# Kernel optimization log

Hardware: AMD Instinct MI355X
Metric: run time of the kernel (lower is better)

The kernel has to match this reference:

```python
import jax, jax.numpy as jnp
import numpy as np

NEG_SLOPE = 0.2
EPS = 1e-6
K = 16


def vec_lna(x, Wf, Wd):
    # x: (B, Cin, 3, ...). Vector-neuron linear + VN-LeakyReLU.
    p = jnp.einsum('oc,bc...->bo...', Wf, x)          # features (B, Cout, 3, ...)
    d = jnp.einsum('oc,bc...->bo...', Wd, x)          # directions (B, Cd, 3, ...), Cd=Cout or 1 (shared)
    dot = jnp.sum(p * d, axis=2, keepdims=True)
    dsq = jnp.sum(d * d, axis=2, keepdims=True)
    p_ref = p - (dot / (dsq + EPS)) * d               # reflect negative part onto hyperplane
    return NEG_SLOPE * p + (1.0 - NEG_SLOPE) * jnp.where(dot >= 0, p, p_ref)


def knn_idx_fn(pts, k):
    # pts: (B, N, 3) -> (B, N, k) indices of k nearest neighbors (incl. self)
    sq = jnp.sum(pts * pts, axis=-1)                  # (B, N)
    d2 = sq[:, :, None] + sq[:, None, :] - 2.0 * jnp.einsum('bnd,bmd->bnm', pts, pts)
    _, idx = jax.lax.top_k(-d2, k)                    # smallest distances
    return idx


def graph_feature(x, idx):
    # x: (B, C, 3, N), idx: (B, N, k) -> (B, 2C, 3, N, k)
    nb = jax.vmap(lambda xb, ib: xb[:, :, ib])(x, idx)  # (B, C, 3, N, k)
    xc = x[..., None]
    return jnp.concatenate([nb - xc, jnp.broadcast_to(xc, nb.shape)], axis=1)


def _winit(key, co, ci):
    return jax.random.normal(key, (co, ci), dtype=jnp.float32) * np.sqrt(2.0 / ci).astype(np.float32)


def setup_inputs() -> dict:
    key = jax.random.key(0)
    ks = jax.random.split(key, 16)
    B, N = 4, 2048
    x = jax.random.normal(ks[0], (B, 3, N), dtype=jnp.float32)
    return {
        'x': x,
        'w1f': _winit(ks[1], 16, 2),   'w1d': _winit(ks[2], 16, 2),
        'w2f': _winit(ks[3], 32, 32),  'w2d': _winit(ks[4], 32, 32),
        'w3f': _winit(ks[5], 64, 64),  'w3d': _winit(ks[6], 64, 64),
        'w4f': _winit(ks[7], 128, 128),'w4d': _winit(ks[8], 128, 128),
        'wcf': _winit(ks[9], 128, 240),'wcd': _winit(ks[10], 1, 240),   # shared nonlinearity -> 1 dir channel
        'wi1f': _winit(ks[11], 128, 256), 'wi1d': _winit(ks[12], 128, 256),
        'wi2f': _winit(ks[13], 256, 128), 'wi2d': _winit(ks[14], 256, 128),
    }


def reference(x, w1f, w1d, w2f, w2d, w3f, w3d, w4f, w4d, wcf, wcd, wi1f, wi1d, wi2f, wi2d):
    # x: (B, 3, N)
    pts = jnp.transpose(x, (0, 2, 1))                 # (B, N, 3)
    idx = knn_idx_fn(pts, K)                          # (B, N, K) -- fixed graph (use_dg=False)
    h = x[:, None]                                    # (B, 1, 3, N)
    h = vec_lna(graph_feature(h, idx), w1f, w1d)
    x1 = h.mean(axis=-1)                              # (B, 16, 3, N)
    h = vec_lna(graph_feature(x1, idx), w2f, w2d)
    x2 = h.mean(axis=-1)                              # (B, 32, 3, N)
    h = vec_lna(graph_feature(x2, idx), w3f, w3d)
    x3 = h.mean(axis=-1)                              # (B, 64, 3, N)
    h = vec_lna(graph_feature(x3, idx), w4f, w4d)
    x4 = h.mean(axis=-1)                              # (B, 128, 3, N)
    xc = vec_lna(jnp.concatenate([x1, x2, x3, x4], axis=1), wcf, wcd)  # (B, 128, 3, N)
    xm = jnp.broadcast_to(xc.mean(axis=-1, keepdims=True), xc.shape)
    xcat = jnp.concatenate([xc, xm], axis=1)          # (B, 256, 3, N)
    x0 = vec_lna(vec_lna(xcat, wi1f, wi1d), wi2f, wi2d)
    inv = jnp.sum(xcat * x0, axis=2)                  # (B, 256, N) rotation-invariant features
    return inv
```

## Files before the change

### kernel.cpp

```cpp
#include <hip/hip_runtime.h>
#include <hip/hip_fp16.h>

#define NPTS  2048
#define BATCH 4
#define NBP   8192
#define MROWS 24576
#define KNN_K 16

typedef short bf16x8 __attribute__((ext_vector_type(8)));
typedef float f32x4  __attribute__((ext_vector_type(4)));

static __device__ __forceinline__ void split_bf16(float a, unsigned short& h, unsigned short& l)
{
    unsigned u = __float_as_uint(a);
    unsigned hr = (u + 0x7FFFu + ((u >> 16) & 1u)) & 0xFFFF0000u;
    h = (unsigned short)(hr >> 16);
    float rem = a - __uint_as_float(hr);
    unsigned v = __float_as_uint(rem);
    l = (unsigned short)((v + 0x7FFFu + ((v >> 16) & 1u)) >> 16);
}

static __device__ __forceinline__ float bf2(unsigned short h, unsigned short l)
{
    return __uint_as_float((unsigned)h << 16) + __uint_as_float((unsigned)l << 16);
}

static __device__ __forceinline__ float lna_scale(float dot, float dsq)
{
    return (dot < 0.f) ? 0.8f * dot * __builtin_amdgcn_rcpf(dsq + 1e-6f) : 0.f;
}

static __device__ __forceinline__ unsigned long long shfl_xor_u64(unsigned long long v, int mask)
{
    unsigned lo = (unsigned)v, hi = (unsigned)(v >> 32);
    lo = (unsigned)__shfl_xor((int)lo, mask, 64);
    hi = (unsigned)__shfl_xor((int)hi, mask, 64);
    return ((unsigned long long)hi << 32) | lo;
}

static __device__ __forceinline__ int xcd_swizzle(int i, int G)
{
    int batch  = (i >> 1) & 3;
    int within = ((i >> 3) << 1) | (i & 1);
    return batch * (G >> 2) + within;
}

static __device__ __forceinline__ float wbig_val(const float* __restrict__ Wf,
                                                 const float* __restrict__ Wd,
                                                 int j, int c, int O, int C)
{
    if (j < 2 * O) {
        int o = j >> 1;
        return (j & 1) ? Wd[o * 2 * C + c] : Wf[o * 2 * C + c];
    }
    int o = (j - 2 * O) >> 1;
    return (j & 1) ? (Wd[o * 2 * C + C + c] - Wd[o * 2 * C + c])
                   : (Wf[o * 2 * C + C + c] - Wf[o * 2 * C + c]);
}

static __device__ __forceinline__ int frag_ix(int r, int c, int RB)
{
    return (((c >> 5) * RB + (r >> 4)) * 64 + ((c >> 3) & 3) * 16 + (r & 15)) * 8 + (c & 7);
}

#define PC0 1572864
#define PC1 (PC0 + 4096)
#define PC2 (PC1 + 8192)
#define PC3 (PC2 + 32768)
#define PC4 (PC3 + 49152)
#define PC5 (PC4 + 32768)
#define PC6 (PC5 + 65536)
#define KNN_BLOCKS (NBP / 4)
#define PREP_BLOCKS (PC6 / 256)

__global__ __launch_bounds__(256) void prep_knn_kernel(
    const float* __restrict__ x, int* __restrict__ idx,
    __half* __restrict__ AH, float* __restrict__ AG,
    const float* __restrict__ w1f, const float* __restrict__ w1d,
    const float* __restrict__ w2f, const float* __restrict__ w2d,
    unsigned short* __restrict__ Wb2h, unsigned short* __restrict__ Wb2l,
    const float* __restrict__ w3f, const float* __restrict__ w3d,
    unsigned short* __restrict__ Wb3h, unsigned short* __restrict__ Wb3l,
    const float* __restrict__ w4f, const float* __restrict__ w4d,
    unsigned short* __restrict__ Wb4h, unsigned short* __restrict__ Wb4l,
    const float* __restrict__ wcf, const float* __restrict__ wcd,
    unsigned short* __restrict__ Wch, unsigned short* __restrict__ Wcl,
    const float* __restrict__ wi1f, const float* __restrict__ wi1d,
    unsigned short* __restrict__ Wi1h, unsigned short* __restrict__ Wi1l,
    const float* __restrict__ wi2f, const float* __restrict__ wi2d,
    unsigned short* __restrict__ Wi2h, unsigned short* __restrict__ Wi2l)
{
    __shared__ unsigned ksh[4][64 * 34];
    if (blockIdx.x < KNN_BLOCKS) {
        const int t  = threadIdx.x & 63;
        const int wq = threadIdx.x >> 6;
        const int bn = blockIdx.x * 4 + wq;
        const int b = bn >> 11;
        const int n = bn & (NPTS - 1);
        const float* xb = x + b * 3 * NPTS;
        const float qx = xb[n], qy = xb[NPTS + n], qz = xb[2 * NPTS + n];
        const float sqn = fmaf(qz, qz, fmaf(qy, qy, qx * qx));
        unsigned* ks = &ksh[wq][t * 34];

        unsigned gm[4];
        int ga[4];
#pragma unroll
        for (int g = 0; g < 4; g++) {
            unsigned kk[8];
#pragma unroll
            for (int j = 0; j < 8; j++) {
                const int i = g * 8 + j;
                const int m = (i << 6) + t;
                float mx = xb[m], my = xb[NPTS + m], mz = xb[2 * NPTS + m];
                float sqm = fmaf(mz, mz, fmaf(my, my, mx * mx));
                float dt  = fmaf(qz, mz, fmaf(qy, my, qx * mx));
                float d2  = sqn + sqm - 2.0f * dt;
                unsigned u = __float_as_uint(d2);
                u ^= (u & 0x80000000u) ? 0xFFFFFFFFu : 0x80000000u;
                kk[j] = u;
            }
            *(uint2*)&ks[g * 8 + 0] = make_uint2(kk[0], kk[1]);
            *(uint2*)&ks[g * 8 + 2] = make_uint2(kk[2], kk[3]);
            *(uint2*)&ks[g * 8 + 4] = make_uint2(kk[4], kk[5]);
            *(uint2*)&ks[g * 8 + 6] = make_uint2(kk[6], kk[7]);
            unsigned bg = kk[0];
            int ba = g * 8;
#pragma unroll
            for (int j = 1; j < 8; j++) {
                if (kk[j] < bg) { bg = kk[j]; ba = g * 8 + j; }
            }
            gm[g] = bg; ga[g] = ba;
        }
        unsigned lm = gm[0];
        int il = ga[0];
#pragma unroll
        for (int g = 1; g < 4; g++) if (gm[g] < lm) { lm = gm[g]; il = ga[g]; }

        unsigned long long pk = ((unsigned long long)lm << 32) | (unsigned)((il << 6) | t);
        int res = -1;
        for (int r = 0; r < KNN_K; r++) {
            unsigned long long w = pk;
#pragma unroll
            for (int off = 32; off > 0; off >>= 1) {
                unsigned long long o = shfl_xor_u64(w, off);
                w = (o < w) ? o : w;
            }
            if (t == r) res = (int)(w & 0xFFFFFFFFull);

            if (pk == w) {
                ks[il] = 0xFFFFFFFFu;
                const int g = il >> 3;
                unsigned bg = ks[g * 8];
                int ba = g * 8;
#pragma unroll
                for (int j = 1; j < 8; j++) {
                    unsigned kv = ks[g * 8 + j];
                    if (kv < bg) { bg = kv; ba = g * 8 + j; }
                }
                gm[g] = bg; ga[g] = ba;
                lm = gm[0]; il = ga[0];
#pragma unroll
                for (int g2 = 1; g2 < 4; g2++) if (gm[g2] < lm) { lm = gm[g2]; il = ga[g2]; }
                pk = ((unsigned long long)lm << 32) | (unsigned)((il << 6) | t);
            }
        }
        if (t < KNN_K) idx[bn * KNN_K + t] = res;
        return;
    }

    const int i = (blockIdx.x - KNN_BLOCKS) * 256 + threadIdx.x;
    if (i < PC0) {
        int o = i & 63;
        int row = i >> 6;
        int v = row % 3;
        int gp = row / 3;
        int b = gp >> 11;
        int n = gp & (NPTS - 1);
        float xv = x[(b * 3 + v) * NPTS + n];
        float wv = wbig_val(w1f, w1d, o, 0, 16, 1);
        float val = xv * wv;
        if (o < 32) AH[(size_t)row * 32 + o] = __float2half(val);
        else        AG[(size_t)row * 32 + o - 32] = val;
    } else if (i < PC6) {
        float v = 0.f;
        unsigned short *ph, *pl;
        int ix;
        if (i < PC1) {
            ix = i - PC0;
            int c = ix & 31, j = ix >> 5;
            if (c < 16) v = wbig_val(w2f, w2d, j, c, 32, 16);
            ph = Wb2h; pl = Wb2l;
        } else if (i < PC2) {
            ix = i - PC1;
            int c = ix & 31, j = ix >> 5;
            v = wbig_val(w3f, w3d, j, c, 64, 32);
            ph = Wb3h; pl = Wb3l;
        } else if (i < PC3) {
            ix = i - PC2;
            int c = ix & 63, j = ix >> 6;
            v = wbig_val(w4f, w4d, j, c, 128, 64);
            ph = Wb4h; pl = Wb4l;
        } else if (i < PC4) {
            ix = i - PC3;
            int c = ix & 255, r = ix >> 8;
            if (c < 240) {
                if (r < 128) v = wcf[r * 240 + c];
                else if (r < 129) v = wcd[(r - 128) * 240 + c];
            }
            ph = Wch; pl = Wcl;
            ix = frag_ix(r, c, 12);
        } else if (i < PC5) {
            ix = i - PC4;
            int c = ix & 127, r = ix >> 7;
            if (r < 128) v = wi1f[r * 256 + c];
            else v = wi1d[(r - 128) * 256 + c];
            ph = Wi1h; pl = Wi1l;
            ix = frag_ix(r, c, 16);
        } else {
            ix = i - PC5;
            int c = ix & 127, r = ix >> 7;
            int o = r >> 1;
            v = (r & 1) ? wi2d[o * 128 + c] : wi2f[o * 128 + c];
            ph = Wi2h; pl = Wi2l;
            ix = frag_ix(r, c, 32);
        }
        unsigned short h, l;
        split_bf16(v, h, l);
        ph[ix] = h; pl[ix] = l;
    }
}

template <int OIN, int NF>
__global__ __launch_bounds__(256, 3) void edge_gemm_kernel(
    const __half* __restrict__ AHin, const float* __restrict__ AGin,
    const int* __restrict__ idx,
    unsigned short* __restrict__ X240h, unsigned short* __restrict__ X240l, int ooff,
    const unsigned short* __restrict__ Wh, const unsigned short* __restrict__ Wl,
    __half* __restrict__ OUTA, float* __restrict__ OUTG)
{
    constexpr int PTS = 16;
    constexpr int NC = NF * 64;
    constexpr int twoO = NC / 2;
    constexpr int LDW = 40;
    constexpr int CPT = OIN / 16;
    constexpr int twoOin = 2 * OIN;

    __shared__ unsigned short Xsh[48][32];
    __shared__ unsigned short Xsl[48][32];
    __shared__ unsigned short wbh[NC][LDW];
    __shared__ unsigned short wbl[NC][LDW];
    __shared__ int sIdx[PTS][KNN_K];

    const int lb = xcd_swizzle(blockIdx.x, gridDim.x);
    const int tid = threadIdx.x;

    for (int rr = tid; rr < NC; rr += 256) {
#pragma unroll
        for (int scc = 0; scc < 4; scc++) {
            *(uint4*)&wbh[rr][scc * 8] = *(const uint4*)(Wh + (size_t)rr * 32 + scc * 8);
            *(uint4*)&wbl[rr][scc * 8] = *(const uint4*)(Wl + (size_t)rr * 32 + scc * 8);
        }
    }
    for (int j = tid; j < PTS * KNN_K; j += 256)
        sIdx[j >> 4][j & 15] = idx[(lb * PTS + (j >> 4)) * KNN_K + (j & 15)];
    __syncthreads();

    const int op = tid & 15;
    const int pt = tid >> 4;
    const int gp = lb * PTS + pt;
    const int b = gp >> 11;
    const int rown = gp * 3;
    const int bbase = (b << 11) * 3;

    float cg[3][2 * CPT];
#pragma unroll
    for (int v = 0; v < 3; v++) {
        if constexpr (CPT == 2) {
            float4 c4 = *(const float4*)&AGin[(size_t)(rown + v) * twoOin + 4 * op];
            cg[v][0] = c4.x; cg[v][1] = c4.y; cg[v][2] = c4.z; cg[v][3] = c4.w;
        } else {
            float2 c2 = *(const float2*)&AGin[(size_t)(rown + v) * twoOin + 2 * op];
            cg[v][0] = c2.x; cg[v][1] = c2.y;
        }
    }
    float am[CPT][3];
#pragma unroll
    for (int c0 = 0; c0 < CPT; c0++) { am[c0][0] = 0.f; am[c0][1] = 0.f; am[c0][2] = 0.f; }

#pragma unroll 2
    for (int k = 0; k < KNN_K; k++) {
        const int m = sIdx[pt][k];
        const __half* base = AHin + (size_t)(bbase + m * 3) * twoOin + 2 * CPT * op;
        float e[3][2 * CPT];
#pragma unroll
        for (int v = 0; v < 3; v++) {
            if constexpr (CPT == 2) {
                uint2 u = *(const uint2*)(base + (size_t)v * twoOin);
                float2 x0 = __half22float2(*(__half2*)&u.x);
                float2 x1 = __half22float2(*(__half2*)&u.y);
                e[v][0] = x0.x; e[v][1] = x0.y; e[v][2] = x1.x; e[v][3] = x1.y;
            } else {
                unsigned u = *(const unsigned*)(base + (size_t)v * twoOin);
                float2 x0 = __half22float2(*(__half2*)&u);
                e[v][0] = x0.x; e[v][1] = x0.y;
            }
        }
#pragma unroll
        for (int c0 = 0; c0 < CPT; c0++) {
            float p0 = e[0][2 * c0] + cg[0][2 * c0], d0 = e[0][2 * c0 + 1] + cg[0][2 * c0 + 1];
            float p1 = e[1][2 * c0] + cg[1][2 * c0], d1 = e[1][2 * c0 + 1] + cg[1][2 * c0 + 1];
            float p2 = e[2][2 * c0] + cg[2][2 * c0], d2 = e[2][2 * c0 + 1] + cg[2][2 * c0 + 1];
            float dot = fmaf(p2, d2, fmaf(p1, d1, p0 * d0));
            float dsq = fmaf(d2, d2, fmaf(d1, d1, d0 * d0));
            float s = lna_scale(dot, dsq);
            am[c0][0] += fmaf(-s, d0, p0);
            am[c0][1] += fmaf(-s, d1, p1);
            am[c0][2] += fmaf(-s, d2, p2);
        }
    }

#pragma unroll
    for (int v = 0; v < 3; v++) {
#pragma unroll
        for (int c0 = 0; c0 < CPT; c0++) {
            const int ch = CPT * op + c0;
            unsigned short h, l;
            split_bf16(am[c0][v] * 0.0625f, h, l);
            Xsh[pt * 3 + v][ch] = h;
            Xsl[pt * 3 + v][ch] = l;
            const size_t ob = (size_t)(rown + v) * 256 + ooff + ch;
            X240h[ob] = h; X240l[ob] = l;
        }
        if constexpr (CPT == 1) {
            Xsh[pt * 3 + v][16 + op] = 0;
            Xsl[pt * 3 + v][16 + op] = 0;
        }
    }
    __syncthreads();

    const int lane = tid & 63;
    const int wv = tid >> 6;
    const int mr = lane & 15;
    const int q  = lane >> 4;

    f32x4 acc[3][NF];
#pragma unroll
    for (int a = 0; a < 3; a++)
#pragma unroll
        for (int c = 0; c < NF; c++) acc[a][c] = (f32x4){0.f, 0.f, 0.f, 0.f};

    bf16x8 ah[3], al[3], bh[NF], bl[NF];
#pragma unroll
    for (int mf = 0; mf < 3; mf++) {
        ah[mf] = *(const bf16x8*)&Xsh[mf * 16 + mr][q * 8];
        al[mf] = *(const bf16x8*)&Xsl[mf * 16 + mr][q * 8];
    }
#pragma unroll
    for (int nf = 0; nf < NF; nf++) {
        const int wr = wv * 16 * NF + nf * 16 + mr;
        bh[nf] = *(const bf16x8*)&wbh[wr][q * 8];
        bl[nf] = *(const bf16x8*)&wbl[wr][q * 8];
    }
#pragma unroll
    for (int mf = 0; mf < 3; mf++)
#pragma unroll
        for (int nf = 0; nf < NF; nf++) {
            acc[mf][nf] = __builtin_amdgcn_mfma_f32_16x16x32_bf16(ah[mf], bh[nf], acc[mf][nf], 0, 0, 0);
            acc[mf][nf] = __builtin_amdgcn_mfma_f32_16x16x32_bf16(ah[mf], bl[nf], acc[mf][nf], 0, 0, 0);
            acc[mf][nf] = __builtin_amdgcn_mfma_f32_16x16x32_bf16(al[mf], bh[nf], acc[mf][nf], 0, 0, 0);
        }

    const int rbase = lb * 48;
#pragma unroll
    for (int nf = 0; nf < NF; nf++) {
        const int col = wv * 16 * NF + nf * 16 + mr;
#pragma unroll
        for (int mf = 0; mf < 3; mf++)
#pragma unroll
            for (int i = 0; i < 4; i++) {
                const int row = rbase + mf * 16 + q * 4 + i;
                const float val = acc[mf][nf][i];
                if (col < twoO) OUTA[(size_t)row * twoO + col] = __float2half(val);
                else            OUTG[(size_t)row * twoO + col - twoO] = val;
            }
    }
}

__global__ __launch_bounds__(256) void gemm_mfma(
    const unsigned short* __restrict__ Xh, const unsigned short* __restrict__ Xl,
    int ldx, int xoff,
    const unsigned short* __restrict__ Wh, const unsigned short* __restrict__ Wl,
    float* __restrict__ OUT, int ldo, int Nout, int Kpad,
    __half* __restrict__ OUTA, float* __restrict__ OUTG, int twoO)
{
    __shared__ unsigned short Ws[2][64][56];
    const int tid = threadIdx.x;
    const int bm = blockIdx.x * 256;
    const int bo = blockIdx.y * 64;
    const int lane = tid & 63;
    const int wv = tid >> 6;
    const int mr = lane & 15;
    const int q  = lane >> 4;

    f32x4 acc[4][4];
#pragma unroll
    for (int a = 0; a < 4; a++)
#pragma unroll
        for (int c = 0; c < 4; c++) acc[a][c] = (f32x4){0.f, 0.f, 0.f, 0.f};

    const int wr = tid >> 2;
    const int sc = tid & 3;

    for (int k0 = 0; k0 < Kpad; k0 += 32) {
        {
            const uint4 vh = *(const uint4*)(Wh + (size_t)(bo + wr) * Kpad + k0 + sc * 8);
            const uint4 vl = *(const uint4*)(Wl + (size_t)(bo + wr) * Kpad + k0 + sc * 8);
            *(uint4*)&Ws[0][wr][sc * 8] = vh;
            *(uint4*)&Ws[1][wr][sc * 8] = vl;
        }
        __syncthreads();

        bf16x8 ah[4], al[4], bh[4], bl[4];
#pragma unroll
        for (int mf = 0; mf < 4; mf++) {
            const size_t xrow = (size_t)(bm + wv * 64 + mf * 16 + mr) * ldx + xoff + k0 + q * 8;
            ah[mf] = *(const bf16x8*)(Xh + xrow);
            al[mf] = *(const bf16x8*)(Xl + xrow);
        }
#pragma unroll
        for (int nf = 0; nf < 4; nf++) {
            bh[nf] = *(const bf16x8*)&Ws[0][nf * 16 + mr][q * 8];
            bl[nf] = *(const bf16x8*)&Ws[1][nf * 16 + mr][q * 8];
        }
#pragma unroll
        for (int mf = 0; mf < 4; mf++)
#pragma unroll
            for (int nf = 0; nf < 4; nf++) {
                acc[mf][nf] = __builtin_amdgcn_mfma_f32_16x16x32_bf16(ah[mf], bh[nf], acc[mf][nf], 0, 0, 0);
                acc[mf][nf] = __builtin_amdgcn_mfma_f32_16x16x32_bf16(ah[mf], bl[nf], acc[mf][nf], 0, 0, 0);
                acc[mf][nf] = __builtin_amdgcn_mfma_f32_16x16x32_bf16(al[mf], bh[nf], acc[mf][nf], 0, 0, 0);
            }
        __syncthreads();
    }

    if (OUTA) {
#pragma unroll
        for (int nf = 0; nf < 4; nf++) {
            const int col = bo + nf * 16 + mr;
            if (col < twoO) {
#pragma unroll
                for (int mf = 0; mf < 4; mf++)
#pragma unroll
                    for (int i = 0; i < 4; i++) {
                        const int row = bm + wv * 64 + mf * 16 + q * 4 + i;
                        OUTA[(size_t)row * twoO + col] = __float2half(acc[mf][nf][i]);
                    }
            } else {
#pragma unroll
                for (int mf = 0; mf < 4; mf++)
#pragma unroll
                    for (int i = 0; i < 4; i++) {
                        const int row = bm + wv * 64 + mf * 16 + q * 4 + i;
                        OUTG[(size_t)row * twoO + col - twoO] = acc[mf][nf][i];
                    }
            }
        }
    } else {
#pragma unroll
        for (int nf = 0; nf < 4; nf++) {
            const int col = bo + nf * 16 + mr;
            if (col < Nout) {
#pragma unroll
                for (int mf = 0; mf < 4; mf++)
#pragma unroll
                    for (int i = 0; i < 4; i++) {
                        const int row = bm + wv * 64 + mf * 16 + q * 4 + i;
                        OUT[(size_t)row * ldo + col] = acc[mf][nf][i];
                    }
            }
        }
    }
}

template <int O, int PT>
__global__ __launch_bounds__(256, 6) void edge_kernel(const __half* __restrict__ AH,
                                                      const float* __restrict__ AG,
                                                      const int* __restrict__ idx,
                                                      unsigned short* __restrict__ outh,
                                                      unsigned short* __restrict__ outl,
                                                      int ooff)
{
    constexpr int TP = O / 2;
    constexpr int twoO = 2 * O;
    const int lb = xcd_swizzle(blockIdx.x, gridDim.x);
    const int tid = threadIdx.x;
    const int op = tid % TP;
    const int pt = tid / TP;
    const int gp = lb * PT + pt;
    const int b = gp >> 11;
    __shared__ int sIdx[PT][KNN_K];
    for (int j = tid; j < PT * KNN_K; j += 256)
        sIdx[j >> 4][j & 15] = idx[(lb * PT + (j >> 4)) * KNN_K + (j & 15)];
    __syncthreads();
    const int rown = gp * 3;
    const float4 c0 = *(const float4*)&AG[(size_t)(rown + 0) * twoO + 4 * op];
    const float4 c1 = *(const float4*)&AG[(size_t)(rown + 1) * twoO + 4 * op];
    const float4 c2 = *(const float4*)&AG[(size_t)(rown + 2) * twoO + 4 * op];
    float ax0 = 0.f, ax1 = 0.f, ax2 = 0.f;
    float ay0 = 0.f, ay1 = 0.f, ay2 = 0.f;
    const int bbase = (b << 11) * 3;
#pragma unroll 2
    for (int k = 0; k < KNN_K; k++) {
        int m = sIdx[pt][k];
        const __half* base = AH + (size_t)(bbase + m * 3) * twoO + 4 * op;
        uint2 u0 = *(const uint2*)(base);
        uint2 u1 = *(const uint2*)(base + twoO);
        uint2 u2 = *(const uint2*)(base + 2 * twoO);
        float2 e0 = __half22float2(*(__half2*)&u0.x);
        float2 f0 = __half22float2(*(__half2*)&u0.y);
        float2 e1 = __half22float2(*(__half2*)&u1.x);
        float2 f1 = __half22float2(*(__half2*)&u1.y);
        float2 e2 = __half22float2(*(__half2*)&u2.x);
        float2 f2 = __half22float2(*(__half2*)&u2.y);
        {
            float p0 = e0.x + c0.x, d0 = e0.y + c0.y;
            float p1 = e1.x + c1.x, d1 = e1.y + c1.y;
            float p2 = e2.x + c2.x, d2 = e2.y + c2.y;
            float dot = fmaf(p2, d2, fmaf(p1, d1, p0 * d0));
            float dsq = fmaf(d2, d2, fmaf(d1, d1, d0 * d0));
            float s = lna_scale(dot, dsq);
            ax0 += fmaf(-s, d0, p0);
            ax1 += fmaf(-s, d1, p1);
            ax2 += fmaf(-s, d2, p2);
        }
        {
            float p0 = f0.x + c0.z, d0 = f0.y + c0.w;
            float p1 = f1.x + c1.z, d1 = f1.y + c1.w;
            float p2 = f2.x + c2.z, d2 = f2.y + c2.w;
            float dot = fmaf(p2, d2, fmaf(p1, d1, p0 * d0));
            float dsq = fmaf(d2, d2, fmaf(d1, d1, d0 * d0));
            float s = lna_scale(dot, dsq);
            ay0 += fmaf(-s, d0, p0);
            ay1 += fmaf(-s, d1, p1);
            ay2 += fmaf(-s, d2, p2);
        }
    }
    float rx[3] = { ax0 * 0.0625f, ax1 * 0.0625f, ax2 * 0.0625f };
    float ry[3] = { ay0 * 0.0625f, ay1 * 0.0625f, ay2 * 0.0625f };
#pragma unroll
    for (int v = 0; v < 3; v++) {
        unsigned short hx, lx, hy, ly;
        split_bf16(rx[v], hx, lx);
        split_bf16(ry[v], hy, ly);
        const size_t ob = (size_t)(rown + v) * 256 + ooff + 2 * op;
        *(unsigned*)(outh + ob) = (unsigned)hx | ((unsigned)hy << 16);
        *(unsigned*)(outl + ob) = (unsigned)lx | ((unsigned)ly << 16);
    }
}

#define EW_LDX 136
#define EW_LDT 133
__global__ __launch_bounds__(256, 4) void edge_wc_kernel(
    const __half* __restrict__ AHin, const float* __restrict__ AGin,
    const int* __restrict__ idx,
    const unsigned short* __restrict__ Xh, const unsigned short* __restrict__ Xl,
    const unsigned short* __restrict__ Wh, const unsigned short* __restrict__ Wl,
    unsigned short* __restrict__ oh, unsigned short* __restrict__ ol,
    float* __restrict__ part2)
{
    __shared__ __align__(16) char smem[48 * EW_LDX * 2 * 2];
    unsigned short (*x4h)[EW_LDX] = (unsigned short (*)[EW_LDX])smem;
    unsigned short (*x4l)[EW_LDX] = (unsigned short (*)[EW_LDX])(smem + 48 * EW_LDX * 2);
    float* tb = (float*)smem;
    __shared__ int sIdx[16][KNN_K];

    const int lb = xcd_swizzle(blockIdx.x, gridDim.x);
    const int tid = threadIdx.x;

    for (int j = tid; j < 16 * KNN_K; j += 256)
        sIdx[j >> 4][j & 15] = idx[(lb * 16 + (j >> 4)) * KNN_K + (j & 15)];
    __syncthreads();

    {
        const int op = tid & 15;
        const int pt = tid >> 4;
        const int gp = lb * 16 + pt;
        const int b = gp >> 11;
        const int rown = gp * 3;
        const int bbase = (b << 11) * 3;

        float cg[3][16];
#pragma unroll
        for (int v = 0; v < 3; v++) {
            const float* ag = &AGin[(size_t)(rown + v) * 256 + 16 * op];
#pragma unroll
            for (int t = 0; t < 4; t++) {
                float4 c4 = *(const float4*)(ag + 4 * t);
                cg[v][4 * t + 0] = c4.x; cg[v][4 * t + 1] = c4.y;
                cg[v][4 * t + 2] = c4.z; cg[v][4 * t + 3] = c4.w;
            }
        }
        float am[8][3];
#pragma unroll
        for (int c0 = 0; c0 < 8; c0++) { am[c0][0] = 0.f; am[c0][1] = 0.f; am[c0][2] = 0.f; }

        for (int k = 0; k < KNN_K; k++) {
            const int m = sIdx[pt][k];
            const __half* base = AHin + (size_t)(bbase + m * 3) * 256 + 16 * op;
            unsigned uw[3][8];
#pragma unroll
            for (int v = 0; v < 3; v++) {
                uint4 a  = *(const uint4*)(base + (size_t)v * 256);
                uint4 bq = *(const uint4*)(base + (size_t)v * 256 + 8);
                uw[v][0] = a.x;  uw[v][1] = a.y;  uw[v][2] = a.z;  uw[v][3] = a.w;
                uw[v][4] = bq.x; uw[v][5] = bq.y; uw[v][6] = bq.z; uw[v][7] = bq.w;
            }
#pragma unroll
            for (int c0 = 0; c0 < 8; c0++) {
                float2 e0 = __half22float2(*(__half2*)&uw[0][c0]);
                float2 e1 = __half22float2(*(__half2*)&uw[1][c0]);
                float2 e2 = __half22float2(*(__half2*)&uw[2][c0]);
                float p0 = e0.x + cg[0][2 * c0], d0 = e0.y + cg[0][2 * c0 + 1];
                float p1 = e1.x + cg[1][2 * c0], d1 = e1.y + cg[1][2 * c0 + 1];
                float p2 = e2.x + cg[2][2 * c0], d2 = e2.y + cg[2][2 * c0 + 1];
                float dot = fmaf(p2, d2, fmaf(p1, d1, p0 * d0));
                float dsq = fmaf(d2, d2, fmaf(d1, d1, d0 * d0));
                float s = lna_scale(dot, dsq);
                am[c0][0] += fmaf(-s, d0, p0);
                am[c0][1] += fmaf(-s, d1, p1);
                am[c0][2] += fmaf(-s, d2, p2);
            }
        }
#pragma unroll
        for (int v = 0; v < 3; v++)
#pragma unroll
            for (int c0 = 0; c0 < 8; c0++) {
                unsigned short h, l;
                split_bf16(am[c0][v] * 0.0625f, h, l);
                x4h[pt * 3 + v][8 * op + c0] = h;
                x4l[pt * 3 + v][8 * op + c0] = l;
            }
    }
    __syncthreads();

    const int lane = tid & 63;
    const int wv = tid >> 6;
    const int mr = lane & 15;
    const int q  = lane >> 4;
    const int rbase = lb * 48;

    f32x4 acc[3][3];
#pragma unroll
    for (int a = 0; a < 3; a++)
#pragma unroll
        for (int c = 0; c < 3; c++) acc[a][c] = (f32x4){0.f, 0.f, 0.f, 0.f};

    for (int k0 = 0; k0 < 256; k0 += 32) {
        const int kb = k0 + q * 8;
        bf16x8 ah[3], al[3], bh[3], bl[3];
#pragma unroll
        for (int mf = 0; mf < 3; mf++) {
            const int row = mf * 16 + mr;
            if (kb >= 112) {
                if (kb >= 240) {
                    ah[mf] = (bf16x8){0, 0, 0, 0, 0, 0, 0, 0};
                    al[mf] = (bf16x8){0, 0, 0, 0, 0, 0, 0, 0};
                } else {
                    ah[mf] = *(const bf16x8*)&x4h[row][kb - 112];
                    al[mf] = *(const bf16x8*)&x4l[row][kb - 112];
                }
            } else {
                const size_t xr = (size_t)(rbase + row) * 256 + kb;
                ah[mf] = *(const bf16x8*)(Xh + xr);
                al[mf] = *(const bf16x8*)(Xl + xr);
            }
        }
#pragma unroll
        for (int nf = 0; nf < 3; nf++) {
            const size_t wri = (size_t)((((k0 >> 5) * 12) + wv * 3 + nf) * 64 + lane) * 8;
            bh[nf] = *(const bf16x8*)(Wh + wri);
            bl[nf] = *(const bf16x8*)(Wl + wri);
        }
#pragma unroll
        for (int mf = 0; mf < 3; mf++)
#pragma unroll
            for (int nf = 0; nf < 3; nf++) {
                acc[mf][nf] = __builtin_amdgcn_mfma_f32_16x16x32_bf16(ah[mf], bh[nf], acc[mf][nf], 0, 0, 0);
                acc[mf][nf] = __builtin_amdgcn_mfma_f32_16x16x32_bf16(ah[mf], bl[nf], acc[mf][nf], 0, 0, 0);
                acc[mf][nf] = __builtin_amdgcn_mfma_f32_16x16x32_bf16(al[mf], bh[nf], acc[mf][nf], 0, 0, 0);
            }
    }
    __syncthreads();

#pragma unroll
    for (int mf = 0; mf < 3; mf++)
#pragma unroll
        for (int nf = 0; nf < 3; nf++) {
            const int col = wv * 48 + nf * 16 + mr;
            if (col <= 128) {
#pragma unroll
                for (int i = 0; i < 4; i++)
                    tb[(mf * 16 + q * 4 + i) * EW_LDT + col] = acc[mf][nf][i];
            }
        }
    __syncthreads();

    const int bp0 = lb * 16;
    float vacc[3] = {0.f, 0.f, 0.f};
#pragma unroll
    for (int it = 0; it < 8; it++) {
        const int item = it * 256 + tid;
        const int o = item & 127;
        const int pt = item >> 7;
        float p[3], d[3];
#pragma unroll
        for (int v = 0; v < 3; v++) {
            const int r = pt * 3 + v;
            p[v] = tb[r * EW_LDT + o];
            d[v] = tb[r * EW_LDT + 128];
        }
        float dot = fmaf(p[2], d[2], fmaf(p[1], d[1], p[0] * d[0]));
        float dsq = fmaf(d[2], d[2], fmaf(d[1], d[1], d[0] * d[0]));
        float s = lna_scale(dot, dsq);
#pragma unroll
        for (int v = 0; v < 3; v++) {
            float val = fmaf(-s, d[v], p[v]);
            vacc[v] += val;
            unsigned short h, l;
            split_bf16(val, h, l);
            const size_t ob = ((size_t)(bp0 + pt) * 3 + v) * 128 + o;
            oh[ob] = h; ol[ob] = l;
        }
    }

    __syncthreads();
    tb[tid] = vacc[0]; tb[256 + tid] = vacc[1]; tb[512 + tid] = vacc[2];
    __syncthreads();
    if (tid < 128) {
#pragma unroll
        for (int v = 0; v < 3; v++)
            part2[(size_t)lb * 384 + v * 128 + tid] =
                tb[v * 256 + tid] + tb[v * 256 + tid + 128];
    }
}

__global__ __launch_bounds__(128) void xm_reduce_ym_kernel(
    const float* __restrict__ part2,
    unsigned short* __restrict__ xmh, unsigned short* __restrict__ xml,
    const float* __restrict__ wi1f, const float* __restrict__ wi1d,
    float* __restrict__ ym)
{
    __shared__ float xs[128];
    const int bv = blockIdx.x;
    const int b = bv / 3;
    const int v = bv % 3;
    const int o = threadIdx.x;
    float acc = 0.f;
    for (int i = 0; i < 128; i++)
        acc += part2[(size_t)(b * 128 + i) * 384 + v * 128 + o];
    const float m = acc * (1.f / 2048.f);
    unsigned short h, l;
    split_bf16(m, h, l);
    xmh[bv * 128 + o] = h;
    xml[bv * 128 + o] = l;
    xs[o] = m;
    __syncthreads();
#pragma unroll
    for (int half = 0; half < 2; half++) {
        const int oo = half * 128 + o;
        const float* wrow = (oo < 128) ? (wi1f + (size_t)oo * 256 + 128)
                                       : (wi1d + (size_t)(oo - 128) * 256 + 128);
        float s = 0.f;
        for (int c = 0; c < 128; c++) s = fmaf(wrow[c], xs[c], s);
        ym[(size_t)bv * 256 + oo] = s;
    }
}

#define QI_LDY  136
#define QI_LDT  257
#define QI_LDT2 67
__global__ __launch_bounds__(256, 2) void gemm_ii_kernel(
    const unsigned short* __restrict__ xch, const unsigned short* __restrict__ xcl,
    const unsigned short* __restrict__ W1h, const unsigned short* __restrict__ W1l,
    const unsigned short* __restrict__ W2h, const unsigned short* __restrict__ W2l,
    const unsigned short* __restrict__ xmh, const unsigned short* __restrict__ xml,
    const float* __restrict__ ym,
    float* __restrict__ out)
{
    __shared__ __align__(16) char regA[51456];
    __shared__ __align__(16) unsigned short y1h[48][QI_LDY];
    __shared__ __align__(16) unsigned short y1l[48][QI_LDY];
    float* tb = (float*)regA;

    const int tid = threadIdx.x;
    const int lane = tid & 63;
    const int wv = tid >> 6;
    const int mr = lane & 15;
    const int q  = lane >> 4;
    const int lb = blockIdx.x;
    const int bm = lb * 48;
    const int bb = (lb * 16) >> 11;

    f32x4 acc[3][4];
#pragma unroll
    for (int a = 0; a < 3; a++)
#pragma unroll
        for (int c = 0; c < 4; c++) acc[a][c] = (f32x4){0.f, 0.f, 0.f, 0.f};

    for (int k0 = 0; k0 < 128; k0 += 32) {
        bf16x8 ah[3], al[3];
#pragma unroll
        for (int mf = 0; mf < 3; mf++) {
            const size_t xr = (size_t)(bm + mf * 16 + mr) * 128 + k0 + q * 8;
            ah[mf] = *(const bf16x8*)(xch + xr);
            al[mf] = *(const bf16x8*)(xcl + xr);
        }
        const int ks = k0 >> 5;
#pragma unroll
        for (int nf = 0; nf < 4; nf++) {
            const size_t wi = (size_t)((ks * 16 + wv * 4 + nf) * 64 + lane) * 8;
            const bf16x8 bh = *(const bf16x8*)(W1h + wi);
            const bf16x8 bl = *(const bf16x8*)(W1l + wi);
#pragma unroll
            for (int mf = 0; mf < 3; mf++) {
                acc[mf][nf] = __builtin_amdgcn_mfma_f32_16x16x32_bf16(ah[mf], bh, acc[mf][nf], 0, 0, 0);
                acc[mf][nf] = __builtin_amdgcn_mfma_f32_16x16x32_bf16(ah[mf], bl, acc[mf][nf], 0, 0, 0);
                acc[mf][nf] = __builtin_amdgcn_mfma_f32_16x16x32_bf16(al[mf], bh, acc[mf][nf], 0, 0, 0);
            }
        }
    }

#pragma unroll
    for (int mf = 0; mf < 3; mf++)
#pragma unroll
        for (int nf = 0; nf < 4; nf++)
#pragma unroll
            for (int i = 0; i < 4; i++)
                tb[(size_t)(mf * 16 + q * 4 + i) * QI_LDT + wv * 64 + nf * 16 + mr] = acc[mf][nf][i];
    __syncthreads();

    {
        const int oo = tid & 127;
        float ymp[3], ymd[3];
#pragma unroll
        for (int v = 0; v < 3; v++) {
            ymp[v] = ym[(size_t)(bb * 3 + v) * 256 + oo];
            ymd[v] = ym[(size_t)(bb * 3 + v) * 256 + 128 + oo];
        }
#pragma unroll
        for (int it = 0; it < 8; it++) {
            const int item = it * 256 + tid;
            const int o = item & 127;
            const int pt = item >> 7;
            float p[3], d[3];
#pragma unroll
            for (int v = 0; v < 3; v++) {
                const int r = pt * 3 + v;
                p[v] = tb[(size_t)r * QI_LDT + o] + ymp[v];
                d[v] = tb[(size_t)r * QI_LDT + 128 + o] + ymd[v];
            }
            float dot = fmaf(p[2], d[2], fmaf(p[1], d[1], p[0] * d[0]));
            float dsq = fmaf(d[2], d[2], fmaf(d[1], d[1], d[0] * d[0]));
            float s = lna_scale(dot, dsq);
#pragma unroll
            for (int v = 0; v < 3; v++) {
                unsigned short h, l;
                split_bf16(fmaf(-s, d[v], p[v]), h, l);
                y1h[pt * 3 + v][o] = h;
                y1l[pt * 3 + v][o] = l;
            }
        }
    }
    __syncthreads();

    f32x4 acc2[3][8];
#pragma unroll
    for (int a = 0; a < 3; a++)
#pragma unroll
        for (int c = 0; c < 8; c++) acc2[a][c] = (f32x4){0.f, 0.f, 0.f, 0.f};

    for (int k0 = 0; k0 < 128; k0 += 32) {
        bf16x8 ah[3], al[3];
#pragma unroll
        for (int mf = 0; mf < 3; mf++) {
            ah[mf] = *(const bf16x8*)&y1h[mf * 16 + mr][k0 + q * 8];
            al[mf] = *(const bf16x8*)&y1l[mf * 16 + mr][k0 + q * 8];
        }
#pragma unroll
        for (int nf = 0; nf < 8; nf++) {
            const size_t wi = (size_t)((((k0 >> 5) * 32) + wv * 8 + nf) * 64 + lane) * 8;
            const bf16x8 bh = *(const bf16x8*)(W2h + wi);
            const bf16x8 bl = *(const bf16x8*)(W2l + wi);
#pragma unroll
            for (int mf = 0; mf < 3; mf++) {
                acc2[mf][nf] = __builtin_amdgcn_mfma_f32_16x16x32_bf16(ah[mf], bh, acc2[mf][nf], 0, 0, 0);
                acc2[mf][nf] = __builtin_amdgcn_mfma_f32_16x16x32_bf16(ah[mf], bl, acc2[mf][nf], 0, 0, 0);
                acc2[mf][nf] = __builtin_amdgcn_mfma_f32_16x16x32_bf16(al[mf], bh, acc2[mf][nf], 0, 0, 0);
            }
        }
    }

    float* wt = tb + wv * (48 * QI_LDT2);
#pragma unroll
    for (int hf = 0; hf < 2; hf++) {
        __syncthreads();
#pragma unroll
        for (int mf = 0; mf < 3; mf++)
#pragma unroll
            for (int nf2 = 0; nf2 < 4; nf2++)
#pragma unroll
                for (int i = 0; i < 4; i++)
                    wt[(mf * 16 + q * 4 + i) * QI_LDT2 + nf2 * 16 + mr] = acc2[mf][hf * 4 + nf2][i];
#pragma unroll
        for (int j = 0; j < 8; j++) {
            const int item = j * 64 + lane;
            const int ol = item & 31;
            const int pt = item >> 5;
            const int og = wv * 64 + hf * 32 + ol;
            const int gp = lb * 16 + pt;
            float p[3], d[3], xc[3];
#pragma unroll
            for (int v = 0; v < 3; v++) {
                p[v] = wt[(3 * pt + v) * QI_LDT2 + 2 * ol];
                d[v] = wt[(3 * pt + v) * QI_LDT2 + 2 * ol + 1];
                if (og < 128) {
                    const size_t ix = (size_t)(gp * 3 + v) * 128 + og;
                    xc[v] = bf2(xch[ix], xcl[ix]);
                } else {
                    const size_t ix = (size_t)(bb * 3 + v) * 128 + og - 128;
                    xc[v] = bf2(xmh[ix], xml[ix]);
                }
            }
            float dot = fmaf(p[2], d[2], fmaf(p[1], d[1], p[0] * d[0]));
            float dsq = fmaf(d[2], d[2], fmaf(d[1], d[1], d[0] * d[0]));
            float s = lna_scale(dot, dsq);
            float inv = 0.f;
#pragma unroll
            for (int v = 0; v < 3; v++)
                inv = fmaf(xc[v], fmaf(-s, d[v], p[v]), inv);
            out[((size_t)bb * 256 + og) * NPTS + (gp & (NPTS - 1))] = inv;
        }
    }
}

extern "C" void kernel_launch(void* const* d_in, const int* in_sizes, int n_in,
                              void* d_out, int out_size, void* d_ws, size_t ws_size,
                              hipStream_t stream)
{
    const float* x    = (const float*)d_in[0];
    const float* w1f  = (const float*)d_in[1];
    const float* w1d  = (const float*)d_in[2];
    const float* w2f  = (const float*)d_in[3];
    const float* w2d  = (const float*)d_in[4];
    const float* w3f  = (const float*)d_in[5];
    const float* w3d  = (const float*)d_in[6];
    const float* w4f  = (const float*)d_in[7];
    const float* w4d  = (const float*)d_in[8];
    const float* wcf  = (const float*)d_in[9];
    const float* wcd  = (const float*)d_in[10];
    const float* wi1f = (const float*)d_in[11];
    const float* wi1d = (const float*)d_in[12];
    const float* wi2f = (const float*)d_in[13];
    const float* wi2d = (const float*)d_in[14];
    float* out = (float*)d_out;

    float* F = (float*)d_ws;
    size_t off = 0;
    float* AG = F + off;                          off += (size_t)MROWS * 512;
    __half* AH = (__half*)(F + off);              off += (size_t)MROWS * 128;
    __half* AH2 = (__half*)(F + off);             off += (size_t)MROWS * 128;
    unsigned short* X240h = (unsigned short*)(F + off); off += (size_t)MROWS * 128;
    unsigned short* X240l = (unsigned short*)(F + off); off += (size_t)MROWS * 128;
    unsigned short* xc2h  = (unsigned short*)(F + off); off += (size_t)MROWS * 64;
    unsigned short* xc2l  = (unsigned short*)(F + off); off += (size_t)MROWS * 64;
    unsigned short* Wb2h = (unsigned short*)(F + off); off += 2048;
    unsigned short* Wb2l = (unsigned short*)(F + off); off += 2048;
    unsigned short* Wb3h = (unsigned short*)(F + off); off += 4096;
    unsigned short* Wb3l = (unsigned short*)(F + off); off += 4096;
    unsigned short* Wb4h = (unsigned short*)(F + off); off += 16384;
    unsigned short* Wb4l = (unsigned short*)(F + off); off += 16384;
    unsigned short* Wch  = (unsigned short*)(F + off); off += 24576;
    unsigned short* Wcl  = (unsigned short*)(F + off); off += 24576;
    unsigned short* Wi1h = (unsigned short*)(F + off); off += 32768;
    unsigned short* Wi1l = (unsigned short*)(F + off); off += 32768;
    unsigned short* Wi2h = (unsigned short*)(F + off); off += 32768;
    unsigned short* Wi2l = (unsigned short*)(F + off); off += 32768;
    float* part2 = F + off;                       off += (size_t)512 * 384;
    float* ym    = F + off;                       off += 12 * 256;
    unsigned short* xmph = (unsigned short*)(F + off); off += 768;
    unsigned short* xmpl = (unsigned short*)(F + off); off += 768;
    int* idx    = (int*)(F + off);                off += NBP * KNN_K;
    float* AG2 = AG + (size_t)MROWS * 256;

    prep_knn_kernel<<<KNN_BLOCKS + PREP_BLOCKS, 256, 0, stream>>>(
        x, idx, AH, AG, w1f, w1d,
        w2f, w2d, Wb2h, Wb2l, w3f, w3d, Wb3h, Wb3l, w4f, w4d, Wb4h, Wb4l,
        wcf, wcd, Wch, Wcl, wi1f, wi1d, Wi1h, Wi1l, wi2f, wi2d, Wi2h, Wi2l);

    const int GM = MROWS / 256;

    edge_gemm_kernel<16, 2><<<NBP / 16, 256, 0, stream>>>(
        AH, AG, idx, X240h, X240l, 0, Wb2h, Wb2l, AH2, AG2);
    edge_gemm_kernel<32, 4><<<NBP / 16, 256, 0, stream>>>(
        AH2, AG2, idx, X240h, X240l, 16, Wb3h, Wb3l, AH, AG);
    edge_kernel<64, 8><<<NBP / 8, 256, 0, stream>>>(AH, AG, idx, X240h, X240l, 48);
    gemm_mfma<<<dim3(GM, 8), 256, 0, stream>>>(X240h, X240l, 256, 48, Wb4h, Wb4l, nullptr, 0, 512, 64, AH2, AG2, 256);

    edge_wc_kernel<<<NBP / 16, 256, 0, stream>>>(AH2, AG2, idx, X240h, X240l,
                                                 Wch, Wcl, xc2h, xc2l, part2);

    xm_reduce_ym_kernel<<<BATCH * 3, 128, 0, stream>>>(part2, xmph, xmpl, wi1f, wi1d, ym);

    gemm_ii_kernel<<<MROWS / 48, 256, 0, stream>>>(xc2h, xc2l, Wi1h, Wi1l,
                                                   Wi2h, Wi2l, xmph, xmpl, ym, out);

    (void)in_sizes; (void)n_in; (void)out_size; (void)ws_size;
}
```

Measured before the change: 252.0 us.

## Fuse layer-3 edge aggregation with layer-4 projection GEMM into one kernel

Replaces the separate edge_kernel<64,8> and gemm_mfma launches with a single edge_gemm4_kernel. Each block aggregates 16 points' neighbor features into shared memory as split bf16 and then runs the 512-wide MFMA projection directly from LDS. The Wb4 weights are pre-laid-out in fragment order so each lane loads B fragments straight from global memory. This removes one launch and the global round-trip of the aggregated features before the GEMM. In exchange it raises register pressure (24 accumulators per lane, launch bounds of 2) and re-reads the weights from global memory in every block.

```diff
diff --git a/kernel.cpp b/kernel.cpp
--- a/kernel.cpp
+++ b/kernel.cpp
@@ -197,9 +197,10 @@
             ph = Wb3h; pl = Wb3l;
         } else if (i < PC3) {
             ix = i - PC2;
-            int c = ix & 63, j = ix >> 6;
-            v = wbig_val(w4f, w4d, j, c, 128, 64);
+            int c = ix & 63, r = ix >> 6;
+            v = wbig_val(w4f, w4d, r, c, 128, 64);
             ph = Wb4h; pl = Wb4l;
+            ix = frag_ix(r, c, 32);
         } else if (i < PC4) {
             ix = i - PC3;
             int c = ix & 255, r = ix >> 8;
@@ -386,175 +387,130 @@
     }
 }
 
-__global__ __launch_bounds__(256) void gemm_mfma(
-    const unsigned short* __restrict__ Xh, const unsigned short* __restrict__ Xl,
-    int ldx, int xoff,
+__global__ __launch_bounds__(256, 2) void edge_gemm4_kernel(
+    const __half* __restrict__ AHin, const float* __restrict__ AGin,
+    const int* __restrict__ idx,
+    unsigned short* __restrict__ X240h, unsigned short* __restrict__ X240l,
     const unsigned short* __restrict__ Wh, const unsigned short* __restrict__ Wl,
-    float* __restrict__ OUT, int ldo, int Nout, int Kpad,
-    __half* __restrict__ OUTA, float* __restrict__ OUTG, int twoO)
-{
-    __shared__ unsigned short Ws[2][64][56];
+    __half* __restrict__ OUTA, float* __restrict__ OUTG)
+{
+    __shared__ unsigned short Xsh[48][72];
+    __shared__ unsigned short Xsl[48][72];
+    __shared__ int sIdx[16][KNN_K];
+
+    const int lb = xcd_swizzle(blockIdx.x, gridDim.x);
     const int tid = threadIdx.x;
-    const int bm = blockIdx.x * 256;
-    const int bo = blockIdx.y * 64;
+
+    for (int j = tid; j < 16 * KNN_K; j += 256)
+        sIdx[j >> 4][j & 15] = idx[(lb * 16 + (j >> 4)) * KNN_K + (j & 15)];
+    __syncthreads();
+
+    {
+        const int op = tid & 15;
+        const int pt = tid >> 4;
+        const int gp = lb * 16 + pt;
+        const int b = gp >> 11;
+        const int rown = gp * 3;
+        const int bbase = (b << 11) * 3;
+
+        float cg[3][8];
+#pragma unroll
+        for (int v = 0; v < 3; v++) {
+            const float* ag = &AGin[(size_t)(rown + v) * 128 + 8 * op];
+            float4 c4a = *(const float4*)ag;
+            float4 c4b = *(const float4*)(ag + 4);
+            cg[v][0] = c4a.x; cg[v][1] = c4a.y; cg[v][2] = c4a.z; cg[v][3] = c4a.w;
+            cg[v][4] = c4b.x; cg[v][5] = c4b.y; cg[v][6] = c4b.z; cg[v][7] = c4b.w;
+        }
+        float am[4][3];
+#pragma unroll
+        for (int c0 = 0; c0 < 4; c0++) { am[c0][0] = 0.f; am[c0][1] = 0.f; am[c0][2] = 0.f; }
+
+        for (int k = 0; k < KNN_K; k++) {
+            const int m = sIdx[pt][k];
+            const __half* base = AHin + (size_t)(bbase + m * 3) * 128 + 8 * op;
+            unsigned uw[3][4];
+#pragma unroll
+            for (int v = 0; v < 3; v++) {
+                uint4 a = *(const uint4*)(base + (size_t)v * 128);
+                uw[v][0] = a.x; uw[v][1] = a.y; uw[v][2] = a.z; uw[v][3] = a.w;
+            }
+#pragma unroll
+            for (int c0 = 0; c0 < 4; c0++) {
+                float2 e0 = __half22float2(*(__half2*)&uw[0][c0]);
+                float2 e1 = __half22float2(*(__half2*)&uw[1][c0]);
+                float2 e2 = __half22float2(*(__half2*)&uw[2][c0]);
+                float p0 = e0.x + cg[0][2 * c0], d0 = e0.y + cg[0][2 * c0 + 1];
+                float p1 = e1.x + cg[1][2 * c0], d1 = e1.y + cg[1][2 * c0 + 1];
+                float p2 = e2.x + cg[2][2 * c0], d2 = e2.y + cg[2][2 * c0 + 1];
+                float dot = fmaf(p2, d2, fmaf(p1, d1, p0 * d0));
+                float dsq = fmaf(d2, d2, fmaf(d1, d1, d0 * d0));
+                float s = lna_scale(dot, dsq);
+                am[c0][0] += fmaf(-s, d0, p0);
+                am[c0][1] += fmaf(-s, d1, p1);
+                am[c0][2] += fmaf(-s, d2, p2);
+            }
+        }
+#pragma unroll
+        for (int v = 0; v < 3; v++)
+#pragma unroll
+            for (int c0 = 0; c0 < 4; c0++) {
+                const int ch = 4 * op + c0;
+                unsigned short h, l;
+                split_bf16(am[c0][v] * 0.0625f, h, l);
+                Xsh[pt * 3 + v][ch] = h;
+                Xsl[pt * 3 + v][ch] = l;
+                const size_t ob = (size_t)(rown + v) * 256 + 48 + ch;
+                X240h[ob] = h; X240l[ob] = l;
+            }
+    }
+    __syncthreads();
+
     const int lane = tid & 63;
     const int wv = tid >> 6;
     const int mr = lane & 15;
     const int q  = lane >> 4;
 
-    f32x4 acc[4][4];
-#pragma unroll
-    for (int a = 0; a < 4; a++)
-#pragma unroll
-        for (int c = 0; c < 4; c++) acc[a][c] = (f32x4){0.f, 0.f, 0.f, 0.f};
-
-    const int wr = tid >> 2;
-    const int sc = tid & 3;
-
-    for (int k0 = 0; k0 < Kpad; k0 += 32) {
-        {
-            const uint4 vh = *(const uint4*)(Wh + (size_t)(bo + wr) * Kpad + k0 + sc * 8);
-            const uint4 vl = *(const uint4*)(Wl + (size_t)(bo + wr) * Kpad + k0 + sc * 8);
-            *(uint4*)&Ws[0][wr][sc * 8] = vh;
-            *(uint4*)&Ws[1][wr][sc * 8] = vl;
-        }
-        __syncthreads();
-
-        bf16x8 ah[4], al[4], bh[4], bl[4];
-#pragma unroll
-        for (int mf = 0; mf < 4; mf++) {
-            const size_t xrow = (size_t)(bm + wv * 64 + mf * 16 + mr) * ldx + xoff + k0 + q * 8;
-            ah[mf] = *(const bf16x8*)(Xh + xrow);
-            al[mf] = *(const bf16x8*)(Xl + xrow);
-        }
-#pragma unroll
-        for (int nf = 0; nf < 4; nf++) {
-            bh[nf] = *(const bf16x8*)&Ws[0][nf * 16 + mr][q * 8];
-            bl[nf] = *(const bf16x8*)&Ws[1][nf * 16 + mr][q * 8];
-        }
-#pragma unroll
-        for (int mf = 0; mf < 4; mf++)
-#pragma unroll
-            for (int nf = 0; nf < 4; nf++) {
-                acc[mf][nf] = __builtin_amdgcn_mfma_f32_16x16x32_bf16(ah[mf], bh[nf], acc[mf][nf], 0, 0, 0);
-                acc[mf][nf] = __builtin_amdgcn_mfma_f32_16x16x32_bf16(ah[mf], bl[nf], acc[mf][nf], 0, 0, 0);
-                acc[mf][nf] = __builtin_amdgcn_mfma_f32_16x16x32_bf16(al[mf], bh[nf], acc[mf][nf], 0, 0, 0);
-            }
-        __syncthreads();
-    }
-
-    if (OUTA) {
-#pragma unroll
-        for (int nf = 0; nf < 4; nf++) {
-            const int col = bo + nf * 16 + mr;
-            if (col < twoO) {
-#pragma unroll
-                for (int mf = 0; mf < 4; mf++)
-#pragma unroll
-                    for (int i = 0; i < 4; i++) {
-                        const int row = bm + wv * 64 + mf * 16 + q * 4 + i;
-                        OUTA[(size_t)row * twoO + col] = __float2half(acc[mf][nf][i]);
-                    }
-            } else {
-#pragma unroll
-                for (int mf = 0; mf < 4; mf++)
-#pragma unroll
-                    for (int i = 0; i < 4; i++) {
-                        const int row = bm + wv * 64 + mf * 16 + q * 4 + i;
-                        OUTG[(size_t)row * twoO + col - twoO] = acc[mf][nf][i];
-                    }
-            }
-        }
-    } else {
-#pragma unroll
-        for (int nf = 0; nf < 4; nf++) {
-            const int col = bo + nf * 16 + mr;
-            if (col < Nout) {
-#pragma unroll
-                for (int mf = 0; mf < 4; mf++)
-#pragma unroll
-                    for (int i = 0; i < 4; i++) {
-                        const int row = bm + wv * 64 + mf * 16 + q * 4 + i;
-                        OUT[(size_t)row * ldo + col] = acc[mf][nf][i];
-                    }
-            }
-        }
-    }
-}
-
-template <int O, int PT>
-__global__ __launch_bounds__(256, 6) void edge_kernel(const __half* __restrict__ AH,
-                                                      const float* __restrict__ AG,
-                                                      const int* __restrict__ idx,
-                                                      unsigned short* __restrict__ outh,
-                                                      unsigned short* __restrict__ outl,
-                                                      int ooff)
-{
-    constexpr int TP = O / 2;
-    constexpr int twoO = 2 * O;
-    const int lb = xcd_swizzle(blockIdx.x, gridDim.x);
-    const int tid = threadIdx.x;
-    const int op = tid % TP;
-    const int pt = tid / TP;
-    const int gp = lb * PT + pt;
-    const int b = gp >> 11;
-    __shared__ int sIdx[PT][KNN_K];
-    for (int j = tid; j < PT * KNN_K; j += 256)
-        sIdx[j >> 4][j & 15] = idx[(lb * PT + (j >> 4)) * KNN_K + (j & 15)];
-    __syncthreads();
-    const int rown = gp * 3;
-    const float4 c0 = *(const float4*)&AG[(size_t)(rown + 0) * twoO + 4 * op];
-    const float4 c1 = *(const float4*)&AG[(size_t)(rown + 1) * twoO + 4 * op];
-    const float4 c2 = *(const float4*)&AG[(size_t)(rown + 2) * twoO + 4 * op];
-    float ax0 = 0.f, ax1 = 0.f, ax2 = 0.f;
-    float ay0 = 0.f, ay1 = 0.f, ay2 = 0.f;
-    const int bbase = (b << 11) * 3;
-#pragma unroll 2
-    for (int k = 0; k < KNN_K; k++) {
-        int m = sIdx[pt][k];
-        const __half* base = AH + (size_t)(bbase + m * 3) * twoO + 4 * op;
-        uint2 u0 = *(const uint2*)(base);
-        uint2 u1 = *(const uint2*)(base + twoO);
-        uint2 u2 = *(const uint2*)(base + 2 * twoO);
-        float2 e0 = __half22float2(*(__half2*)&u0.x);
-        float2 f0 = __half22float2(*(__half2*)&u0.y);
-        float2 e1 = __half22float2(*(__half2*)&u1.x);
-        float2 f1 = __half22float2(*(__half2*)&u1.y);
-        float2 e2 = __half22float2(*(__half2*)&u2.x);
-        float2 f2 = __half22float2(*(__half2*)&u2.y);
-        {
-            float p0 = e0.x + c0.x, d0 = e0.y + c0.y;
-            float p1 = e1.x + c1.x, d1 = e1.y + c1.y;
-            float p2 = e2.x + c2.x, d2 = e2.y + c2.y;
-            float dot = fmaf(p2, d2, fmaf(p1, d1, p0 * d0));
-            float dsq = fmaf(d2, d2, fmaf(d1, d1, d0 * d0));
-            float s = lna_scale(dot, dsq);
-            ax0 += fmaf(-s, d0, p0);
-            ax1 += fmaf(-s, d1, p1);
-            ax2 += fmaf(-s, d2, p2);
-        }
-        {
-            float p0 = f0.x + c0.z, d0 = f0.y + c0.w;
-            float p1 = f1.x + c1.z, d1 = f1.y + c1.w;
-            float p2 = f2.x + c2.z, d2 = f2.y + c2.w;
-            float dot = fmaf(p2, d2, fmaf(p1, d1, p0 * d0));
-            float dsq = fmaf(d2, d2, fmaf(d1, d1, d0 * d0));
-            float s = lna_scale(dot, dsq);
-            ay0 += fmaf(-s, d0, p0);
-            ay1 += fmaf(-s, d1, p1);
-            ay2 += fmaf(-s, d2, p2);
-        }
-    }
-    float rx[3] = { ax0 * 0.0625f, ax1 * 0.0625f, ax2 * 0.0625f };
-    float ry[3] = { ay0 * 0.0625f, ay1 * 0.0625f, ay2 * 0.0625f };
-#pragma unroll
-    for (int v = 0; v < 3; v++) {
-        unsigned short hx, lx, hy, ly;
-        split_bf16(rx[v], hx, lx);
-        split_bf16(ry[v], hy, ly);
-        const size_t ob = (size_t)(rown + v) * 256 + ooff + 2 * op;
-        *(unsigned*)(outh + ob) = (unsigned)hx | ((unsigned)hy << 16);
-        *(unsigned*)(outl + ob) = (unsigned)lx | ((unsigned)ly << 16);
+    f32x4 acc[3][8];
+#pragma unroll
+    for (int a = 0; a < 3; a++)
+#pragma unroll
+        for (int c = 0; c < 8; c++) acc[a][c] = (f32x4){0.f, 0.f, 0.f, 0.f};
+
+    for (int ks = 0; ks < 2; ks++) {
+        bf16x8 ah[3], al[3];
+#pragma unroll
+        for (int mf = 0; mf < 3; mf++) {
+            ah[mf] = *(const bf16x8*)&Xsh[mf * 16 + mr][ks * 32 + q * 8];
+            al[mf] = *(const bf16x8*)&Xsl[mf * 16 + mr][ks * 32 + q * 8];
+        }
+#pragma unroll
+        for (int nf = 0; nf < 8; nf++) {
+            const size_t wi = (size_t)((ks * 32 + wv * 8 + nf) * 64 + lane) * 8;
+            const bf16x8 bh = *(const bf16x8*)(Wh + wi);
+            const bf16x8 bl = *(const bf16x8*)(Wl + wi);
+#pragma unroll
+            for (int mf = 0; mf < 3; mf++) {
+                acc[mf][nf] = __builtin_amdgcn_mfma_f32_16x16x32_bf16(ah[mf], bh, acc[mf][nf], 0, 0, 0);
+                acc[mf][nf] = __builtin_amdgcn_mfma_f32_16x16x32_bf16(ah[mf], bl, acc[mf][nf], 0, 0, 0);
+                acc[mf][nf] = __builtin_amdgcn_mfma_f32_16x16x32_bf16(al[mf], bh, acc[mf][nf], 0, 0, 0);
+            }
+        }
+    }
+
+    const int rbase = lb * 48;
+#pragma unroll
+    for (int nf = 0; nf < 8; nf++) {
+        const int col = wv * 128 + nf * 16 + mr;
+#pragma unroll
+        for (int mf = 0; mf < 3; mf++)
+#pragma unroll
+            for (int i = 0; i < 4; i++) {
+                const int row = rbase + mf * 16 + q * 4 + i;
+                const float val = acc[mf][nf][i];
+                if (col < 256) OUTA[(size_t)row * 256 + col] = __float2half(val);
+                else           OUTG[(size_t)row * 256 + col - 256] = val;
+            }
     }
 }
 
@@ -997,14 +953,12 @@
         w2f, w2d, Wb2h, Wb2l, w3f, w3d, Wb3h, Wb3l, w4f, w4d, Wb4h, Wb4l,
         wcf, wcd, Wch, Wcl, wi1f, wi1d, Wi1h, Wi1l, wi2f, wi2d, Wi2h, Wi2l);
 
-    const int GM = MROWS / 256;
-
     edge_gemm_kernel<16, 2><<<NBP / 16, 256, 0, stream>>>(
         AH, AG, idx, X240h, X240l, 0, Wb2h, Wb2l, AH2, AG2);
     edge_gemm_kernel<32, 4><<<NBP / 16, 256, 0, stream>>>(
         AH2, AG2, idx, X240h, X240l, 16, Wb3h, Wb3l, AH, AG);
-    edge_kernel<64, 8><<<NBP / 8, 256, 0, stream>>>(AH, AG, idx, X240h, X240l, 48);
-    gemm_mfma<<<dim3(GM, 8), 256, 0, stream>>>(X240h, X240l, 256, 48, Wb4h, Wb4l, nullptr, 0, 512, 64, AH2, AG2, 256);
+    edge_gemm4_kernel<<<NBP / 16, 256, 0, stream>>>(
+        AH, AG, idx, X240h, X240l, Wb4h, Wb4l, AH2, AG2);
 
     edge_wc_kernel<<<NBP / 16, 256, 0, stream>>>(AH2, AG2, idx, X240h, X240l,
                                                  Wch, Wcl, xc2h, xc2l, part2);
```

Result: faster. 244.2 us (median of 2 runs) (-3.1%).
